# Optimization experiments

Hardware: AMD Instinct MI355X
Metric: run time of the kernel (lower is better)

Reference implementation:

```python
import jax, jax.numpy as jnp
import numpy as np

N_NODES = 50000


def setup_inputs() -> dict:
    key = jax.random.key(0)
    k1, k2, k3, k4, k5 = jax.random.split(key, 5)
    F_IN, F_OUT, E = 128, 128, 800000
    x = jax.random.normal(k1, (N_NODES, F_IN), dtype=jnp.float32)
    edge_index = jax.random.randint(k2, (2, E), 0, N_NODES, dtype=jnp.int64)
    # PyG Linear uses Kaiming-ish init; scale for stable magnitudes
    s = 1.0 / np.sqrt(F_IN)
    W_l = jax.random.normal(k3, (F_IN, F_OUT), dtype=jnp.float32) * s
    W_r = jax.random.normal(k4, (F_IN, F_OUT), dtype=jnp.float32) * s
    b = jax.random.normal(k5, (F_OUT,), dtype=jnp.float32) * s
    return {"x": x, "edge_index": edge_index, "W_l": W_l, "W_r": W_r, "b": b}


def reference(x, edge_index, W_l, W_r, b):
    # SAGEConv (mean aggr): out = mean_{j in N(i)} x_j @ W_l + x_i @ W_r + b
    src, dst = edge_index[0], edge_index[1]
    msgs = x[src]  # [E, F_in] gather
    summed = jax.ops.segment_sum(msgs, dst, num_segments=N_NODES)  # [N, F_in]
    deg = jax.ops.segment_sum(jnp.ones_like(dst, dtype=x.dtype), dst,
                              num_segments=N_NODES)  # [N]
    mean = summed / jnp.maximum(deg, 1.0)[:, None]
    return mean @ W_l + x @ W_r + b
```

## Files before the change

kernel.cpp:

```cpp
#include <hip/hip_runtime.h>

#define N_NODES 50000
#define F 128
#define NBIN 98
#define BIN_NODES 512
#define BINCAP 10000
#define NB_A 256
#define NB_CV 6250
#define NB_BT 128
#define CGSTRIDE 800000

typedef __attribute__((ext_vector_type(8))) short bf16x8;
typedef __attribute__((ext_vector_type(4))) float f32x4;
typedef __attribute__((ext_vector_type(4))) unsigned int u32x4;

__device__ __forceinline__ unsigned short f2bf(float f) {
    unsigned u = __float_as_uint(f);
    unsigned r = u + 0x7FFFu + ((u >> 16) & 1u);
    return (unsigned short)(r >> 16);
}

__global__ __launch_bounds__(128) void init_kernel(int* __restrict__ cursor)
{
    const int t = threadIdx.x;
    if (t < NBIN) cursor[t] = t * BINCAP;
}

__global__ __launch_bounds__(256) void fused_prep_kernel(
    const float* __restrict__ x, unsigned short* __restrict__ xb,
    unsigned short* __restrict__ xcs,
    const int* __restrict__ src, const int* __restrict__ dst,
    int* __restrict__ cursor, unsigned* __restrict__ binbuf,
    const float* __restrict__ Wl, const float* __restrict__ Wr,
    unsigned short* __restrict__ Bt, int E)
{
    const int bid = blockIdx.x;
    const int t = threadIdx.x;

    if (bid < NB_A) {
        __shared__ int hist[NBIN], hist2[NBIN], base[NBIN];
        if (t < NBIN) { hist[t] = 0; hist2[t] = 0; }
        __syncthreads();

        const int e0 = bid * 3125;
        for (int j = t; j < 3125; j += 256)
            atomicAdd(&hist[dst[e0 + j] >> 9], 1);
        __syncthreads();

        if (t < NBIN) base[t] = atomicAdd(&cursor[t], hist[t]);
        __syncthreads();

        for (int j = t; j < 3125; j += 256) {
            const int d = dst[e0 + j];
            const int s = src[e0 + j];
            const int b = d >> 9;
            const int r = atomicAdd(&hist2[b], 1);
            binbuf[base[b] + r] = (unsigned)s | ((unsigned)(d & 511) << 16);
        }
    } else if (bid < NB_A + NB_CV) {
        const int i = (bid - NB_A) * 256 + t;
        const float4 v = reinterpret_cast<const float4*>(x)[i];
        ushort4 o;
        o.x = f2bf(v.x); o.y = f2bf(v.y); o.z = f2bf(v.z); o.w = f2bf(v.w);
        reinterpret_cast<ushort4*>(xb)[i] = o;
        const int n = i >> 5;
        const int c = i & 31;
        *reinterpret_cast<ushort4*>(
            &xcs[(size_t)(c >> 2) * CGSTRIDE + n * 16 + (c & 3) * 4]) = o;
    } else {
        const int gid = (bid - NB_A - NB_CV) * 256 + t;
        const int n = gid >> 8;
        const int k = gid & 255;
        const float v = (k < F) ? Wl[k * F + n] : Wr[(k - F) * F + n];
        Bt[gid] = f2bf(v);
    }
}

__global__ __launch_bounds__(512) void binscatter_kernel(
    const unsigned* __restrict__ binbuf, const int* __restrict__ cursor,
    unsigned short* __restrict__ csr, int* __restrict__ start,
    int* __restrict__ deg)
{
    __shared__ int degL[BIN_NODES], lofs[BIN_NODES], cnt2[BIN_NODES];
    __shared__ unsigned short lbc[BINCAP];
    __shared__ int wsumS[8];
    __shared__ int pre[128];
    __shared__ int cbaseS;

    const int b = blockIdx.x, t = threadIdx.x;
    const int lane = t & 63, wid = t >> 6;

    degL[t] = 0; cnt2[t] = 0;
    if (t < 128) {
        int v = (t < NBIN) ? (cursor[t] - t * BINCAP) : 0;
        int incl = v;
#pragma unroll
        for (int off = 1; off < 64; off <<= 1) {
            const int u = __shfl_up(incl, off, 64);
            if (lane >= off) incl += u;
        }
        pre[t] = incl;
    }
    __syncthreads();
    if (t == 0)
        cbaseS = (b == 0) ? 0 : ((b <= 64) ? pre[b - 1]
                                           : pre[63] + pre[b - 1]);
    const int lo = b * BINCAP;
    const int hi = cursor[b];
    const int n = hi - lo;

    for (int j = lo + t; j < hi; j += 512)
        atomicAdd(&degL[binbuf[j] >> 16], 1);
    __syncthreads();

    {
        const int v = degL[t];
        int incl = v;
#pragma unroll
        for (int off = 1; off < 64; off <<= 1) {
            const int u = __shfl_up(incl, off, 64);
            if (lane >= off) incl += u;
        }
        if (lane == 63) wsumS[wid] = incl;
        __syncthreads();
        if (t == 0) {
            int run = 0;
#pragma unroll
            for (int w = 0; w < 8; ++w) { const int s = wsumS[w]; wsumS[w] = run; run += s; }
        }
        __syncthreads();
        lofs[t] = wsumS[wid] + incl - v;
    }
    __syncthreads();

    for (int j = lo + t; j < hi; j += 512) {
        const unsigned p = binbuf[j];
        const int dl = p >> 16;
        const int r = atomicAdd(&cnt2[dl], 1);
        lbc[lofs[dl] + r] = (unsigned short)(p & 0xFFFFu);
    }
    __syncthreads();

    const int gn0 = b * BIN_NODES;
    if (gn0 + t < N_NODES) {
        start[gn0 + t] = cbaseS + lofs[t];
        deg[gn0 + t] = degL[t];
    }
    for (int i = t; i < n; i += 512) csr[cbaseS + i] = lbc[i];
}

__global__ __launch_bounds__(256) void agg_sliced_kernel(
    const unsigned short* __restrict__ xcs,
    const unsigned short* __restrict__ csr,
    const int* __restrict__ start,
    const int* __restrict__ deg,
    unsigned short* __restrict__ meancs)
{
    const int cg = blockIdx.x & 7;
    const int chunk = blockIdx.x >> 3;
    const int t = threadIdx.x;
    const int lane = t & 63, w = t >> 6;
    const int g8 = lane >> 3, l8 = lane & 7;
    const int node = chunk * 32 + w * 8 + g8;
    if (node >= N_NODES) return;

    const int s0 = start[node];
    const int d = deg[node];
    const unsigned short* xs = xcs + (size_t)cg * CGSTRIDE;

    int idx0 = (l8      < d) ? (int)csr[s0 + l8]      : 0;
    int idx1 = (l8 + 8  < d) ? (int)csr[s0 + l8 + 8]  : 0;
    int idx2 = (l8 + 16 < d) ? (int)csr[s0 + l8 + 16] : 0;
    int idx3 = (l8 + 24 < d) ? (int)csr[s0 + l8 + 24] : 0;
    int idx4 = (l8 + 32 < d) ? (int)csr[s0 + l8 + 32] : 0;
    int idx5 = (l8 + 40 < d) ? (int)csr[s0 + l8 + 40] : 0;
    int idx6 = (l8 + 48 < d) ? (int)csr[s0 + l8 + 48] : 0;
    int idx7 = (l8 + 56 < d) ? (int)csr[s0 + l8 + 56] : 0;

    float a0 = 0.f, a1 = 0.f;
    const int colu = l8 * 2;
    const int gb = g8 * 8;

#define CHUNK(K, IDX)                                                       \
    if (K * 8 < d) {                                                        \
        const int r0 = __shfl(IDX, gb + 0);                                 \
        const int r1 = __shfl(IDX, gb + 1);                                 \
        const int r2 = __shfl(IDX, gb + 2);                                 \
        const int r3 = __shfl(IDX, gb + 3);                                 \
        const int r4 = __shfl(IDX, gb + 4);                                 \
        const int r5 = __shfl(IDX, gb + 5);                                 \
        const int r6 = __shfl(IDX, gb + 6);                                 \
        const int r7 = __shfl(IDX, gb + 7);                                 \
        const unsigned v0 = *reinterpret_cast<const unsigned*>(&xs[r0 * 16 + colu]); \
        const unsigned v1 = *reinterpret_cast<const unsigned*>(&xs[r1 * 16 + colu]); \
        const unsigned v2 = *reinterpret_cast<const unsigned*>(&xs[r2 * 16 + colu]); \
        const unsigned v3 = *reinterpret_cast<const unsigned*>(&xs[r3 * 16 + colu]); \
        const unsigned v4 = *reinterpret_cast<const unsigned*>(&xs[r4 * 16 + colu]); \
        const unsigned v5 = *reinterpret_cast<const unsigned*>(&xs[r5 * 16 + colu]); \
        const unsigned v6 = *reinterpret_cast<const unsigned*>(&xs[r6 * 16 + colu]); \
        const unsigned v7 = *reinterpret_cast<const unsigned*>(&xs[r7 * 16 + colu]); \
        const int rem = d - K * 8;                                          \
        a0 += __uint_as_float(v0 << 16);                                    \
        a1 += __uint_as_float(v0 & 0xFFFF0000u);                            \
        if (rem > 1) { a0 += __uint_as_float(v1 << 16); a1 += __uint_as_float(v1 & 0xFFFF0000u); } \
        if (rem > 2) { a0 += __uint_as_float(v2 << 16); a1 += __uint_as_float(v2 & 0xFFFF0000u); } \
        if (rem > 3) { a0 += __uint_as_float(v3 << 16); a1 += __uint_as_float(v3 & 0xFFFF0000u); } \
        if (rem > 4) { a0 += __uint_as_float(v4 << 16); a1 += __uint_as_float(v4 & 0xFFFF0000u); } \
        if (rem > 5) { a0 += __uint_as_float(v5 << 16); a1 += __uint_as_float(v5 & 0xFFFF0000u); } \
        if (rem > 6) { a0 += __uint_as_float(v6 << 16); a1 += __uint_as_float(v6 & 0xFFFF0000u); } \
        if (rem > 7) { a0 += __uint_as_float(v7 << 16); a1 += __uint_as_float(v7 & 0xFFFF0000u); } \
    }

    CHUNK(0, idx0)
    CHUNK(1, idx1)
    CHUNK(2, idx2)
    CHUNK(3, idx3)
    CHUNK(4, idx4)
    CHUNK(5, idx5)
    CHUNK(6, idx6)
    CHUNK(7, idx7)
#undef CHUNK

    const float inv = (d > 0) ? (1.0f / (float)d) : 1.0f;
    const unsigned u =
        (unsigned)f2bf(a0 * inv) | ((unsigned)f2bf(a1 * inv) << 16);
    *reinterpret_cast<unsigned*>(
        &meancs[(size_t)cg * CGSTRIDE + node * 16 + colu]) = u;
}

__global__ __launch_bounds__(64) void out_mfma_kernel(
    const unsigned short* __restrict__ meancs,
    const unsigned short* __restrict__ xb,
    const unsigned short* __restrict__ Bt,
    const float* __restrict__ bias,
    float* __restrict__ out)
{
    __shared__ float cs[16][132];

    const int lane = threadIdx.x;
    const int mbase = blockIdx.x * 16;
    const int li = lane & 15, grp = lane >> 4;
    const int arow = mbase + li;
    const int kchunk = grp * 8;

    bf16x8 a[8];
#pragma unroll
    for (int s = 0; s < 4; ++s) {
        const int c0 = s * 32 + kchunk;
        a[s] = *reinterpret_cast<const bf16x8*>(
            &meancs[(size_t)(c0 >> 4) * CGSTRIDE + arow * 16 + (c0 & 15)]);
        a[s + 4] = *reinterpret_cast<const bf16x8*>(
            &xb[(size_t)arow * F + c0]);
    }

    f32x4 acc[8];
#pragma unroll
    for (int nt = 0; nt < 8; ++nt) acc[nt] = (f32x4){0.f, 0.f, 0.f, 0.f};

#pragma unroll
    for (int s = 0; s < 8; ++s) {
#pragma unroll
        for (int nt = 0; nt < 8; ++nt) {
            const bf16x8 bf = *reinterpret_cast<const bf16x8*>(
                &Bt[(size_t)(nt * 16 + li) * 256 + s * 32 + kchunk]);
            acc[nt] = __builtin_amdgcn_mfma_f32_16x16x32_bf16(a[s], bf, acc[nt], 0, 0, 0);
        }
    }

    const int crow_local = grp * 4;
#pragma unroll
    for (int nt = 0; nt < 8; ++nt) {
        const int col = nt * 16 + li;
        const float bv = bias[col];
#pragma unroll
        for (int r = 0; r < 4; ++r)
            cs[crow_local + r][col] = acc[nt][r] + bv;
    }

#pragma unroll
    for (int i = 0; i < 8; ++i) {
        const int idx = lane + i * 64;
        const int r = idx >> 5;
        const int c4 = (idx & 31) << 2;
        float4 v;
        v.x = cs[r][c4 + 0];
        v.y = cs[r][c4 + 1];
        v.z = cs[r][c4 + 2];
        v.w = cs[r][c4 + 3];
        *reinterpret_cast<float4*>(&out[(size_t)(mbase + r) * F + c4]) = v;
    }
}

extern "C" void kernel_launch(void* const* d_in, const int* in_sizes, int n_in,
                              void* d_out, int out_size, void* d_ws, size_t ws_size,
                              hipStream_t stream)
{
    const float* x  = (const float*)d_in[0];
    const int*   ei = (const int*)d_in[1];
    const float* Wl = (const float*)d_in[2];
    const float* Wr = (const float*)d_in[3];
    const float* b  = (const float*)d_in[4];
    float* out = (float*)d_out;

    const int E = in_sizes[1] / 2;
    const int* src = ei;
    const int* dst = ei + E;

    int* cursor = (int*)d_ws;
    int* start  = cursor + 128;
    int* deg    = start + 50176;
    unsigned* binbuf = (unsigned*)(deg + 50176);
    unsigned short* csr    = (unsigned short*)(binbuf + 980000);
    unsigned short* xb     = csr + 800064;
    unsigned short* xcs    = xb + (size_t)N_NODES * F;
    unsigned short* meancs = xcs + (size_t)N_NODES * F;
    unsigned short* Bt     = meancs + (size_t)N_NODES * F;

    init_kernel<<<1, 128, 0, stream>>>(cursor);

    fused_prep_kernel<<<NB_A + NB_CV + NB_BT, 256, 0, stream>>>(
        x, xb, xcs, src, dst, cursor, binbuf, Wl, Wr, Bt, E);

    binscatter_kernel<<<NBIN, 512, 0, stream>>>(binbuf, cursor, csr, start, deg);

    const int nchunk = (N_NODES + 31) / 32;
    agg_sliced_kernel<<<nchunk * 8, 256, 0, stream>>>(
        xcs, csr, start, deg, meancs);

    out_mfma_kernel<<<N_NODES / 16, 64, 0, stream>>>(
        meancs, xb, Bt, b, out);
}
```

Measured before the change: 103.1 us.

## Fuse neighbor mean aggregation into MFMA output kernel, drop column-sliced copy

```diff
diff --git a/kernel.cpp b/kernel.cpp
--- a/kernel.cpp
+++ b/kernel.cpp
@@ -8,7 +8,6 @@
 #define NB_A 256
 #define NB_CV 6250
 #define NB_BT 128
-#define CGSTRIDE 800000
 
 typedef __attribute__((ext_vector_type(8))) short bf16x8;
 typedef __attribute__((ext_vector_type(4))) float f32x4;
@@ -28,7 +27,6 @@
 
 __global__ __launch_bounds__(256) void fused_prep_kernel(
     const float* __restrict__ x, unsigned short* __restrict__ xb,
-    unsigned short* __restrict__ xcs,
     const int* __restrict__ src, const int* __restrict__ dst,
     int* __restrict__ cursor, unsigned* __restrict__ binbuf,
     const float* __restrict__ Wl, const float* __restrict__ Wr,
@@ -63,10 +61,6 @@
         ushort4 o;
         o.x = f2bf(v.x); o.y = f2bf(v.y); o.z = f2bf(v.z); o.w = f2bf(v.w);
         reinterpret_cast<ushort4*>(xb)[i] = o;
-        const int n = i >> 5;
-        const int c = i & 31;
-        *reinterpret_cast<ushort4*>(
-            &xcs[(size_t)(c >> 2) * CGSTRIDE + n * 16 + (c & 3) * 4]) = o;
     } else {
         const int gid = (bid - NB_A - NB_CV) * 256 + t;
         const int n = gid >> 8;
@@ -149,137 +143,113 @@
     for (int i = t; i < n; i += 512) csr[cbaseS + i] = lbc[i];
 }
 
-__global__ __launch_bounds__(256) void agg_sliced_kernel(
-    const unsigned short* __restrict__ xcs,
+__global__ __launch_bounds__(256) void agg_out_kernel(
+    const unsigned short* __restrict__ xb,
     const unsigned short* __restrict__ csr,
     const int* __restrict__ start,
     const int* __restrict__ deg,
-    unsigned short* __restrict__ meancs)
-{
-    const int cg = blockIdx.x & 7;
-    const int chunk = blockIdx.x >> 3;
-    const int t = threadIdx.x;
-    const int lane = t & 63, w = t >> 6;
-    const int g8 = lane >> 3, l8 = lane & 7;
-    const int node = chunk * 32 + w * 8 + g8;
-    if (node >= N_NODES) return;
-
-    const int s0 = start[node];
-    const int d = deg[node];
-    const unsigned short* xs = xcs + (size_t)cg * CGSTRIDE;
-
-    int idx0 = (l8      < d) ? (int)csr[s0 + l8]      : 0;
-    int idx1 = (l8 + 8  < d) ? (int)csr[s0 + l8 + 8]  : 0;
-    int idx2 = (l8 + 16 < d) ? (int)csr[s0 + l8 + 16] : 0;
-    int idx3 = (l8 + 24 < d) ? (int)csr[s0 + l8 + 24] : 0;
-    int idx4 = (l8 + 32 < d) ? (int)csr[s0 + l8 + 32] : 0;
-    int idx5 = (l8 + 40 < d) ? (int)csr[s0 + l8 + 40] : 0;
-    int idx6 = (l8 + 48 < d) ? (int)csr[s0 + l8 + 48] : 0;
-    int idx7 = (l8 + 56 < d) ? (int)csr[s0 + l8 + 56] : 0;
-
-    float a0 = 0.f, a1 = 0.f;
-    const int colu = l8 * 2;
-    const int gb = g8 * 8;
-
-#define CHUNK(K, IDX)                                                       \
-    if (K * 8 < d) {                                                        \
-        const int r0 = __shfl(IDX, gb + 0);                                 \
-        const int r1 = __shfl(IDX, gb + 1);                                 \
-        const int r2 = __shfl(IDX, gb + 2);                                 \
-        const int r3 = __shfl(IDX, gb + 3);                                 \
-        const int r4 = __shfl(IDX, gb + 4);                                 \
-        const int r5 = __shfl(IDX, gb + 5);                                 \
-        const int r6 = __shfl(IDX, gb + 6);                                 \
-        const int r7 = __shfl(IDX, gb + 7);                                 \
-        const unsigned v0 = *reinterpret_cast<const unsigned*>(&xs[r0 * 16 + colu]); \
-        const unsigned v1 = *reinterpret_cast<const unsigned*>(&xs[r1 * 16 + colu]); \
-        const unsigned v2 = *reinterpret_cast<const unsigned*>(&xs[r2 * 16 + colu]); \
-        const unsigned v3 = *reinterpret_cast<const unsigned*>(&xs[r3 * 16 + colu]); \
-        const unsigned v4 = *reinterpret_cast<const unsigned*>(&xs[r4 * 16 + colu]); \
-        const unsigned v5 = *reinterpret_cast<const unsigned*>(&xs[r5 * 16 + colu]); \
-        const unsigned v6 = *reinterpret_cast<const unsigned*>(&xs[r6 * 16 + colu]); \
-        const unsigned v7 = *reinterpret_cast<const unsigned*>(&xs[r7 * 16 + colu]); \
-        const int rem = d - K * 8;                                          \
-        a0 += __uint_as_float(v0 << 16);                                    \
-        a1 += __uint_as_float(v0 & 0xFFFF0000u);                            \
-        if (rem > 1) { a0 += __uint_as_float(v1 << 16); a1 += __uint_as_float(v1 & 0xFFFF0000u); } \
-        if (rem > 2) { a0 += __uint_as_float(v2 << 16); a1 += __uint_as_float(v2 & 0xFFFF0000u); } \
-        if (rem > 3) { a0 += __uint_as_float(v3 << 16); a1 += __uint_as_float(v3 & 0xFFFF0000u); } \
-        if (rem > 4) { a0 += __uint_as_float(v4 << 16); a1 += __uint_as_float(v4 & 0xFFFF0000u); } \
-        if (rem > 5) { a0 += __uint_as_float(v5 << 16); a1 += __uint_as_float(v5 & 0xFFFF0000u); } \
-        if (rem > 6) { a0 += __uint_as_float(v6 << 16); a1 += __uint_as_float(v6 & 0xFFFF0000u); } \
-        if (rem > 7) { a0 += __uint_as_float(v7 << 16); a1 += __uint_as_float(v7 & 0xFFFF0000u); } \
-    }
-
-    CHUNK(0, idx0)
-    CHUNK(1, idx1)
-    CHUNK(2, idx2)
-    CHUNK(3, idx3)
-    CHUNK(4, idx4)
-    CHUNK(5, idx5)
-    CHUNK(6, idx6)
-    CHUNK(7, idx7)
-#undef CHUNK
-
-    const float inv = (d > 0) ? (1.0f / (float)d) : 1.0f;
-    const unsigned u =
-        (unsigned)f2bf(a0 * inv) | ((unsigned)f2bf(a1 * inv) << 16);
-    *reinterpret_cast<unsigned*>(
-        &meancs[(size_t)cg * CGSTRIDE + node * 16 + colu]) = u;
-}
-
-__global__ __launch_bounds__(64) void out_mfma_kernel(
-    const unsigned short* __restrict__ meancs,
-    const unsigned short* __restrict__ xb,
     const unsigned short* __restrict__ Bt,
     const float* __restrict__ bias,
     float* __restrict__ out)
 {
+    __shared__ __align__(16) unsigned short mean_s[16][136];
     __shared__ float cs[16][132];
 
-    const int lane = threadIdx.x;
+    const int t = threadIdx.x;
+    const int w = t >> 6, lane = t & 63;
+    const int li = lane & 15, g = lane >> 4;
     const int mbase = blockIdx.x * 16;
-    const int li = lane & 15, grp = lane >> 4;
+    const int colu = 2 * lane;
+
+#define ACC2(v)                                    \
+    {                                              \
+        a0 += __uint_as_float((v) << 16);          \
+        a1 += __uint_as_float((v) & 0xFFFF0000u);  \
+    }
+
+    for (int q = 0; q < 4; ++q) {
+        const int ln = w * 4 + q;
+        const int node = mbase + ln;
+        const int s0 = start[node];
+        const int d = deg[node];
+
+        const int idx = (lane < d) ? (int)csr[s0 + lane] : 0;
+
+        float a0 = 0.f, a1 = 0.f;
+        for (int j = 0; j < d; j += 8) {
+            const int r0 = __shfl(idx, j + 0);
+            const int r1 = __shfl(idx, j + 1);
+            const int r2 = __shfl(idx, j + 2);
+            const int r3 = __shfl(idx, j + 3);
+            const int r4 = __shfl(idx, j + 4);
+            const int r5 = __shfl(idx, j + 5);
+            const int r6 = __shfl(idx, j + 6);
+            const int r7 = __shfl(idx, j + 7);
+            const unsigned v0 = *reinterpret_cast<const unsigned*>(&xb[(size_t)r0 * F + colu]);
+            const unsigned v1 = *reinterpret_cast<const unsigned*>(&xb[(size_t)r1 * F + colu]);
+            const unsigned v2 = *reinterpret_cast<const unsigned*>(&xb[(size_t)r2 * F + colu]);
+            const unsigned v3 = *reinterpret_cast<const unsigned*>(&xb[(size_t)r3 * F + colu]);
+            const unsigned v4 = *reinterpret_cast<const unsigned*>(&xb[(size_t)r4 * F + colu]);
+            const unsigned v5 = *reinterpret_cast<const unsigned*>(&xb[(size_t)r5 * F + colu]);
+            const unsigned v6 = *reinterpret_cast<const unsigned*>(&xb[(size_t)r6 * F + colu]);
+            const unsigned v7 = *reinterpret_cast<const unsigned*>(&xb[(size_t)r7 * F + colu]);
+            const int rem = d - j;
+            ACC2(v0)
+            if (rem > 1) ACC2(v1)
+            if (rem > 2) ACC2(v2)
+            if (rem > 3) ACC2(v3)
+            if (rem > 4) ACC2(v4)
+            if (rem > 5) ACC2(v5)
+            if (rem > 6) ACC2(v6)
+            if (rem > 7) ACC2(v7)
+        }
+
+        const float inv = (d > 0) ? (1.0f / (float)d) : 1.0f;
+        const unsigned u =
+            (unsigned)f2bf(a0 * inv) | ((unsigned)f2bf(a1 * inv) << 16);
+        *reinterpret_cast<unsigned*>(&mean_s[ln][colu]) = u;
+    }
+#undef ACC2
+    __syncthreads();
+
     const int arow = mbase + li;
-    const int kchunk = grp * 8;
+    const int kchunk = g * 8;
 
     bf16x8 a[8];
 #pragma unroll
     for (int s = 0; s < 4; ++s) {
-        const int c0 = s * 32 + kchunk;
-        a[s] = *reinterpret_cast<const bf16x8*>(
-            &meancs[(size_t)(c0 >> 4) * CGSTRIDE + arow * 16 + (c0 & 15)]);
+        a[s] = *reinterpret_cast<const bf16x8*>(&mean_s[li][s * 32 + kchunk]);
         a[s + 4] = *reinterpret_cast<const bf16x8*>(
-            &xb[(size_t)arow * F + c0]);
-    }
-
-    f32x4 acc[8];
-#pragma unroll
-    for (int nt = 0; nt < 8; ++nt) acc[nt] = (f32x4){0.f, 0.f, 0.f, 0.f};
+            &xb[(size_t)arow * F + s * 32 + kchunk]);
+    }
+
+    f32x4 acc[2];
+    acc[0] = (f32x4){0.f, 0.f, 0.f, 0.f};
+    acc[1] = (f32x4){0.f, 0.f, 0.f, 0.f};
 
 #pragma unroll
     for (int s = 0; s < 8; ++s) {
 #pragma unroll
-        for (int nt = 0; nt < 8; ++nt) {
+        for (int nt = 0; nt < 2; ++nt) {
             const bf16x8 bf = *reinterpret_cast<const bf16x8*>(
-                &Bt[(size_t)(nt * 16 + li) * 256 + s * 32 + kchunk]);
+                &Bt[(size_t)((w * 2 + nt) * 16 + li) * 256 + s * 32 + kchunk]);
             acc[nt] = __builtin_amdgcn_mfma_f32_16x16x32_bf16(a[s], bf, acc[nt], 0, 0, 0);
         }
     }
 
-    const int crow_local = grp * 4;
-#pragma unroll
-    for (int nt = 0; nt < 8; ++nt) {
-        const int col = nt * 16 + li;
+#pragma unroll
+    for (int nt = 0; nt < 2; ++nt) {
+        const int col = (w * 2 + nt) * 16 + li;
         const float bv = bias[col];
 #pragma unroll
         for (int r = 0; r < 4; ++r)
-            cs[crow_local + r][col] = acc[nt][r] + bv;
-    }
-
-#pragma unroll
-    for (int i = 0; i < 8; ++i) {
-        const int idx = lane + i * 64;
+            cs[g * 4 + r][col] = acc[nt][r] + bv;
+    }
+    __syncthreads();
+
+#pragma unroll
+    for (int i = 0; i < 2; ++i) {
+        const int idx = t + i * 256;
         const int r = idx >> 5;
         const int c4 = (idx & 31) << 2;
         float4 v;
@@ -310,23 +280,17 @@
     int* start  = cursor + 128;
     int* deg    = start + 50176;
     unsigned* binbuf = (unsigned*)(deg + 50176);
-    unsigned short* csr    = (unsigned short*)(binbuf + 980000);
-    unsigned short* xb     = csr + 800064;
-    unsigned short* xcs    = xb + (size_t)N_NODES * F;
-    unsigned short* meancs = xcs + (size_t)N_NODES * F;
-    unsigned short* Bt     = meancs + (size_t)N_NODES * F;
+    unsigned short* csr = (unsigned short*)(binbuf + 980000);
+    unsigned short* xb  = csr + 800064;
+    unsigned short* Bt  = xb + (size_t)N_NODES * F;
 
     init_kernel<<<1, 128, 0, stream>>>(cursor);
 
     fused_prep_kernel<<<NB_A + NB_CV + NB_BT, 256, 0, stream>>>(
-        x, xb, xcs, src, dst, cursor, binbuf, Wl, Wr, Bt, E);
+        x, xb, src, dst, cursor, binbuf, Wl, Wr, Bt, E);
 
     binscatter_kernel<<<NBIN, 512, 0, stream>>>(binbuf, cursor, csr, start, deg);
 
-    const int nchunk = (N_NODES + 31) / 32;
-    agg_sliced_kernel<<<nchunk * 8, 256, 0, stream>>>(
-        xcs, csr, start, deg, meancs);
-
-    out_mfma_kernel<<<N_NODES / 16, 64, 0, stream>>>(
-        meancs, xb, Bt, b, out);
-}
+    agg_out_kernel<<<N_NODES / 16, 256, 0, stream>>>(
+        xb, csr, start, deg, Bt, b, out);
+}
```

Measured after the change: 97.27 us. 1.06x faster.
